# Kernel tuning notes

Measured on AMD Instinct MI355X. Metric: run time of the kernel, lower is better.

Reference implementation:

```python
import jax, jax.numpy as jnp
import numpy as np


def setup_inputs() -> dict:
    key = jax.random.key(0)
    k1, k2 = jax.random.split(key)
    B, H, W, N = 32, 1024, 1024, 96
    output = jax.random.uniform(k1, (B, 1, H, W), dtype=jnp.float32)
    bboxes = jax.random.randint(k2, (B, N, 4), 0, W, dtype=jnp.int32)
    return {"output": output, "bboxes": bboxes}


def reference(output, bboxes):
    # output: [B, 1, H, W] density map; bboxes: [B, N, 4] as (x1, y1, x2, y2).
    B, _, H, W = output.shape
    bb = jnp.clip(bboxes.astype(jnp.int32), 0, W)  # torch: bboxes.long().clip(0, W)
    x = output[:, 0]  # [B, H, W]
    # 2D integral image with zero top/left padding: S[b, i, j] = sum of x[b, :i, :j].
    S = jnp.pad(jnp.cumsum(jnp.cumsum(x, axis=1), axis=2), ((0, 0), (1, 0), (1, 0)))  # [B, H+1, W+1]
    x1, y1, x2, y2 = bb[..., 0], bb[..., 1], bb[..., 2], bb[..., 3]  # each [B, N]
    bidx = jnp.arange(B)[:, None]  # [B, 1] broadcast against [B, N]
    g = lambda yy, xx: S[bidx, yy, xx]
    box_sums = g(y2, x2) - g(y1, x2) - g(y2, x1) + g(y1, x1)  # [B, N]
    # Empty torch slices (x2<=x1 or y2<=y1) sum to 0; mask to match.
    valid = (x2 > x1) & (y2 > y1)
    box_sums = jnp.where(valid, box_sums, jnp.zeros_like(box_sums))
    return jnp.sum(jax.nn.relu(1.0 - box_sums))
```

## Files before the change

kernel.cpp:

```cpp
#include <hip/hip_runtime.h>

#define BATCH 32
#define HDIM 1024
#define WDIM 1024
#define NBOX 96
#define ROWS_PER_BLOCK 16
#define THREADS 256

__global__ void zero_ws_kernel(float* __restrict__ ws) {
    int i = blockIdx.x * blockDim.x + threadIdx.x;
    if (i < BATCH * NBOX) ws[i] = 0.0f;
}

__global__ __launch_bounds__(THREADS) void box_accum_kernel(
    const float* __restrict__ img,
    const int* __restrict__ bboxes,
    float* __restrict__ ws_box) {

    __shared__ float Pinc[WDIM];
    __shared__ float wave_tot[THREADS / 64];

    const int t = threadIdx.x;
    const int lane = t & 63;
    const int wave = t >> 6;

    const int blocks_per_batch = HDIM / ROWS_PER_BLOCK;
    const int b = blockIdx.x / blocks_per_batch;
    const int row0 = (blockIdx.x % blocks_per_batch) * ROWS_PER_BLOCK;

    int x1 = 0, y1 = 0, x2 = 0, y2 = 0;
    const bool owns_box = (t < NBOX);
    if (owns_box) {
        const int4 bb = ((const int4*)bboxes)[b * NBOX + t];
        x1 = min(max(bb.x, 0), WDIM);
        y1 = min(max(bb.y, 0), WDIM);
        x2 = min(max(bb.z, 0), WDIM);
        y2 = min(max(bb.w, 0), WDIM);
    }
    const bool x_valid = owns_box && (x2 > x1);
    float acc = 0.0f;

    const float* rowbase = img + ((size_t)b * HDIM + row0) * WDIM;

    for (int r = 0; r < ROWS_PER_BLOCK; ++r) {
        float4 v = ((const float4*)(rowbase + (size_t)r * WDIM))[t];

        float s0 = v.x;
        float s1 = s0 + v.y;
        float s2 = s1 + v.z;
        float s3 = s2 + v.w;

        float wscan = s3;
        #pragma unroll
        for (int off = 1; off < 64; off <<= 1) {
            float u = __shfl_up(wscan, off, 64);
            if (lane >= off) wscan += u;
        }
        float excl_in_wave = wscan - s3;
        if (lane == 63) wave_tot[wave] = wscan;
        __syncthreads();

        float wave_base = 0.0f;
        #pragma unroll
        for (int w = 0; w < THREADS / 64; ++w)
            wave_base += (w < wave) ? wave_tot[w] : 0.0f;

        float base = wave_base + excl_in_wave;

        float4 pv;
        pv.x = base + s0;
        pv.y = base + s1;
        pv.z = base + s2;
        pv.w = base + s3;
        ((float4*)Pinc)[t] = pv;
        __syncthreads();

        const int i = row0 + r;
        if (x_valid && (y1 <= i) && (i < y2)) {
            float right = Pinc[x2 - 1];
            float left  = (x1 > 0) ? Pinc[x1 - 1] : 0.0f;
            acc += right - left;
        }
        __syncthreads();
    }

    if (owns_box && acc != 0.0f) {
        atomicAdd(&ws_box[b * NBOX + t], acc);
    }
}

__global__ void finalize_kernel(const float* __restrict__ ws_box,
                                const int* __restrict__ bboxes,
                                float* __restrict__ out) {
    __shared__ float red[THREADS / 64];
    const int t = threadIdx.x;
    float local = 0.0f;
    for (int idx = t; idx < BATCH * NBOX; idx += THREADS) {
        const int4 bb = ((const int4*)bboxes)[idx];
        int x1 = min(max(bb.x, 0), WDIM);
        int y1 = min(max(bb.y, 0), WDIM);
        int x2 = min(max(bb.z, 0), WDIM);
        int y2 = min(max(bb.w, 0), WDIM);
        bool valid = (x2 > x1) && (y2 > y1);
        float s = valid ? ws_box[idx] : 0.0f;
        local += fmaxf(1.0f - s, 0.0f);
    }
    #pragma unroll
    for (int off = 32; off > 0; off >>= 1)
        local += __shfl_down(local, off, 64);
    if ((t & 63) == 0) red[t >> 6] = local;
    __syncthreads();
    if (t == 0) {
        float r = 0.0f;
        #pragma unroll
        for (int w = 0; w < THREADS / 64; ++w) r += red[w];
        out[0] = r;
    }
}

extern "C" void kernel_launch(void* const* d_in, const int* in_sizes, int n_in,
                              void* d_out, int out_size, void* d_ws, size_t ws_size,
                              hipStream_t stream) {
    const float* img    = (const float*)d_in[0];
    const int*   bboxes = (const int*)d_in[1];
    float* out = (float*)d_out;
    float* ws_box = (float*)d_ws;

    zero_ws_kernel<<<(BATCH * NBOX + THREADS - 1) / THREADS, THREADS, 0, stream>>>(ws_box);

    const int nblocks = BATCH * HDIM / ROWS_PER_BLOCK;
    box_accum_kernel<<<nblocks, THREADS, 0, stream>>>(img, bboxes, ws_box);

    finalize_kernel<<<1, THREADS, 0, stream>>>(ws_box, bboxes, out);
}
```

Baseline: 200.3 us.

## Replace per-row prefix scans with direct per-box region summation

```diff
diff --git a/kernel.cpp b/kernel.cpp
--- a/kernel.cpp
+++ b/kernel.cpp
@@ -4,89 +4,50 @@
 #define HDIM 1024
 #define WDIM 1024
 #define NBOX 96
-#define ROWS_PER_BLOCK 16
 #define THREADS 256
+#define NSLICE 8
 
 __global__ void zero_ws_kernel(float* __restrict__ ws) {
     int i = blockIdx.x * blockDim.x + threadIdx.x;
     if (i < BATCH * NBOX) ws[i] = 0.0f;
 }
 
-__global__ __launch_bounds__(THREADS) void box_accum_kernel(
+__global__ __launch_bounds__(THREADS) void box_direct_kernel(
     const float* __restrict__ img,
     const int* __restrict__ bboxes,
     float* __restrict__ ws_box) {
 
-    __shared__ float Pinc[WDIM];
-    __shared__ float wave_tot[THREADS / 64];
+    const int box = blockIdx.x;
+    const int s   = blockIdx.y;
+    const int b   = box / NBOX;
 
-    const int t = threadIdx.x;
+    const int4 bb = ((const int4*)bboxes)[box];
+    const int x1 = min(max(bb.x, 0), WDIM);
+    const int y1 = min(max(bb.y, 0), WDIM);
+    const int x2 = min(max(bb.z, 0), WDIM);
+    const int y2 = min(max(bb.w, 0), WDIM);
+    if (x2 <= x1 || y2 <= y1) return;
+
+    const int t    = threadIdx.x;
     const int lane = t & 63;
     const int wave = t >> 6;
 
-    const int blocks_per_batch = HDIM / ROWS_PER_BLOCK;
-    const int b = blockIdx.x / blocks_per_batch;
-    const int row0 = (blockIdx.x % blocks_per_batch) * ROWS_PER_BLOCK;
+    const float* base = img + (size_t)b * HDIM * WDIM;
 
-    int x1 = 0, y1 = 0, x2 = 0, y2 = 0;
-    const bool owns_box = (t < NBOX);
-    if (owns_box) {
-        const int4 bb = ((const int4*)bboxes)[b * NBOX + t];
-        x1 = min(max(bb.x, 0), WDIM);
-        y1 = min(max(bb.y, 0), WDIM);
-        x2 = min(max(bb.z, 0), WDIM);
-        y2 = min(max(bb.w, 0), WDIM);
-    }
-    const bool x_valid = owns_box && (x2 > x1);
     float acc = 0.0f;
-
-    const float* rowbase = img + ((size_t)b * HDIM + row0) * WDIM;
-
-    for (int r = 0; r < ROWS_PER_BLOCK; ++r) {
-        float4 v = ((const float4*)(rowbase + (size_t)r * WDIM))[t];
-
-        float s0 = v.x;
-        float s1 = s0 + v.y;
-        float s2 = s1 + v.z;
-        float s3 = s2 + v.w;
-
-        float wscan = s3;
-        #pragma unroll
-        for (int off = 1; off < 64; off <<= 1) {
-            float u = __shfl_up(wscan, off, 64);
-            if (lane >= off) wscan += u;
+    for (int y = y1 + s * 4 + wave; y < y2; y += NSLICE * 4) {
+        const float* row = base + (size_t)y * WDIM;
+        for (int x = x1 + lane; x < x2; x += 64) {
+            acc += row[x];
         }
-        float excl_in_wave = wscan - s3;
-        if (lane == 63) wave_tot[wave] = wscan;
-        __syncthreads();
-
-        float wave_base = 0.0f;
-        #pragma unroll
-        for (int w = 0; w < THREADS / 64; ++w)
-            wave_base += (w < wave) ? wave_tot[w] : 0.0f;
-
-        float base = wave_base + excl_in_wave;
-
-        float4 pv;
-        pv.x = base + s0;
-        pv.y = base + s1;
-        pv.z = base + s2;
-        pv.w = base + s3;
-        ((float4*)Pinc)[t] = pv;
-        __syncthreads();
-
-        const int i = row0 + r;
-        if (x_valid && (y1 <= i) && (i < y2)) {
-            float right = Pinc[x2 - 1];
-            float left  = (x1 > 0) ? Pinc[x1 - 1] : 0.0f;
-            acc += right - left;
-        }
-        __syncthreads();
     }
 
-    if (owns_box && acc != 0.0f) {
-        atomicAdd(&ws_box[b * NBOX + t], acc);
-    }
+    #pragma unroll
+    for (int off = 32; off > 0; off >>= 1)
+        acc += __shfl_xor(acc, off, 64);
+
+    if (lane == 0 && acc != 0.0f)
+        atomicAdd(&ws_box[box], acc);
 }
 
 __global__ void finalize_kernel(const float* __restrict__ ws_box,
@@ -128,8 +89,8 @@
 
     zero_ws_kernel<<<(BATCH * NBOX + THREADS - 1) / THREADS, THREADS, 0, stream>>>(ws_box);
 
-    const int nblocks = BATCH * HDIM / ROWS_PER_BLOCK;
-    box_accum_kernel<<<nblocks, THREADS, 0, stream>>>(img, bboxes, ws_box);
+    dim3 grid(BATCH * NBOX, NSLICE);
+    box_direct_kernel<<<grid, THREADS, 0, stream>>>(img, bboxes, ws_box);
 
     finalize_kernel<<<1, THREADS, 0, stream>>>(ws_box, bboxes, out);
 }
```

Result: slower. 380.4 us (+90.0%).
